# Optimization experiments

Measured on AMD Instinct MI355X. Metric: run time of the kernel, lower is better.

## Reference

```python
import jax, jax.numpy as jnp
import numpy as np

NEG = -1e30  # effective -inf in log space, fp32-safe


def _ctc_loss(logp, labels, label_lens):
    """Sum of per-sequence CTC negative log-likelihoods (blank=0).

    logp: [T, B, V] log-softmax over vocab; labels: [U, B] int (pad=1);
    label_lens: [B]. All sequences use full T frames (act_lens = T).
    """
    T, B, V = logp.shape
    U = labels.shape[0]
    S = 2 * U + 1  # blank-interleaved extended label length
    lab = labels.T  # [B, U]
    ext = jnp.zeros((B, S), dtype=jnp.int32).at[:, 1::2].set(lab.astype(jnp.int32))
    # s-2 transition allowed only for non-blank positions with ext[s] != ext[s-2]
    allow = jnp.concatenate(
        [jnp.zeros((B, 2), bool), (ext[:, 2:] != 0) & (ext[:, 2:] != ext[:, :-2])],
        axis=1,
    )  # [B, S]
    # emission log-probs gathered once: [T, B, S]
    emit = jnp.take_along_axis(logp, jnp.broadcast_to(ext[None], (T, B, S)), axis=2)
    # alpha_0: only s=0 (blank) and s=1 (first label) reachable
    alpha0 = jnp.where(jnp.arange(S)[None, :] < 2, emit[0], NEG)

    def step(alpha, emit_t):
        s1 = jnp.pad(alpha[:, :-1], ((0, 0), (1, 0)), constant_values=NEG)
        s2 = jnp.where(allow, jnp.pad(alpha[:, :-2], ((0, 0), (2, 0)), constant_values=NEG), NEG)
        alpha = jnp.logaddexp(jnp.logaddexp(alpha, s1), s2) + emit_t
        return alpha, None

    alphaT, _ = jax.lax.scan(step, alpha0, emit[1:])
    end = 2 * label_lens  # [B] index of final blank in ext
    idx = jnp.stack([end, end - 1], axis=1)  # [B, 2]
    ll = jax.nn.logsumexp(jnp.take_along_axis(alphaT, idx, axis=1), axis=1)
    return -jnp.sum(ll)  # size_average=False -> sum over batch


def setup_inputs() -> dict:
    T, B, D, NVOC, U = 800, 16, 256, 4000, 100
    V = NVOC + 1  # +1 for blank (index 0)
    key = jax.random.key(0)
    kc, kw, ky, kl = jax.random.split(key, 4)
    ctx = jax.random.normal(kc, (T, B, D), jnp.float32)
    W = jax.random.normal(kw, (D, V), jnp.float32) * 0.02
    b = jnp.zeros((V,), jnp.float32)
    lens = jax.random.randint(kl, (B,), 50, U + 1)
    raw = jax.random.randint(ky, (U, B), 2, V)  # labels in [2, n_vocab]
    y = jnp.where(jnp.arange(U)[:, None] < lens[None, :], raw, 1).astype(jnp.int32)
    return {"ctx": ctx, "y": y, "W": W, "b": b}


def reference(ctx, y, W, b):
    # hid2prob: linear projection to n_vocab+1 logits
    out = jnp.einsum('tbd,dv->tbv', ctx, W) + b  # [T, B, V]
    logps = jax.nn.log_softmax(out, axis=-1)
    label_lens = jnp.sum(y != 1, axis=0)  # pad token is 1
    loss = _ctc_loss(logps, y, label_lens)
    return loss, logps
```

## Files before the change

kernel.cpp:

```cpp
#include <hip/hip_runtime.h>
#include <hip/hip_bf16.h>
#include <stdint.h>

#define T_ 800
#define B_ 16
#define D_ 256
#define V_ 4001
#define U_ 100
#define S_ 201
#define SP 204
#define M_ (T_*B_)
#define NEGF (-1e30f)
#define L2E 1.4426950408889634f
#define LN2 0.6931471805599453f

typedef __bf16 bf16;
typedef __bf16 bf16x8 __attribute__((ext_vector_type(8)));
typedef float f32x4 __attribute__((ext_vector_type(4)));

#define A_OFF     0
#define WT_OFF    6553600
#define EMIT_OFF  8650752
#define EXT_OFF   19095552
#define AMASK_OFF 19108608
#define LENS_OFF  19121664

__global__ void prep_kernel(const int* __restrict__ y, float* __restrict__ out,
                            int* __restrict__ ext, float* __restrict__ amask,
                            int* __restrict__ lens) {
  const int tid = threadIdx.x;
  if (tid == 0) out[0] = 0.f;
  if (tid < B_) {
    int cnt = 0;
    for (int u = 0; u < U_; u++) cnt += (y[u*B_ + tid] != 1) ? 1 : 0;
    lens[tid] = cnt;
  }
  for (int idx = tid; idx < B_*SP; idx += 256) {
    int b = idx / SP, s = idx - b*SP;
    int e = 0;
    if (s < S_ && (s & 1)) e = y[((s-1) >> 1)*B_ + b];
    ext[idx] = e;
    float am = NEGF;
    if ((s & 1) && s >= 3 && s < S_) {
      int e2 = y[((s-3) >> 1)*B_ + b];
      if (e != 0 && e != e2) am = 0.f;
    }
    amask[idx] = am;
  }
}

__global__ void cast_a_kernel(const float* __restrict__ ctx, bf16* __restrict__ A) {
  int i = blockIdx.x * blockDim.x + threadIdx.x;
  float4 v = ((const float4*)ctx)[i];
  union { bf16 h[4]; uint2 u; } p;
  p.h[0] = (bf16)v.x; p.h[1] = (bf16)v.y; p.h[2] = (bf16)v.z; p.h[3] = (bf16)v.w;
  ((uint2*)A)[i] = p.u;
}

__global__ void trans_w_kernel(const float* __restrict__ W, bf16* __restrict__ Wt) {
  __shared__ float tile[32][33];
  const int c = threadIdx.x & 31, r = threadIdx.x >> 5;
  const int n0 = blockIdx.x * 32, k0 = blockIdx.y * 32;
  for (int rr = r; rr < 32; rr += 8) {
    int n = n0 + c;
    tile[rr][c] = (n < V_) ? W[(size_t)(k0+rr)*V_ + n] : 0.f;
  }
  __syncthreads();
  for (int rr = r; rr < 32; rr += 8) {
    Wt[(size_t)(n0+rr)*D_ + k0 + c] = (bf16)tile[c][rr];
  }
}

__global__ __launch_bounds__(256) void gemm_kernel(
    const bf16* __restrict__ A, const bf16* __restrict__ Wt,
    const float* __restrict__ bias, float* __restrict__ out) {
  __shared__ bf16 smA[128*72];
  __shared__ bf16 smB[128*72];
  const int tid = threadIdx.x;
  const int l = tid & 63, w = tid >> 6;
  const int wr = w >> 1, wc = w & 1;
  const int n0 = blockIdx.x * 128, m0 = blockIdx.y * 128;

  f32x4 acc[4][4];
#pragma unroll
  for (int i = 0; i < 4; i++)
#pragma unroll
    for (int j = 0; j < 4; j++) acc[i][j] = (f32x4){0.f, 0.f, 0.f, 0.f};

  for (int kt = 0; kt < 4; kt++) {
#pragma unroll
    for (int r = 0; r < 4; r++) {
      int j = (w*4 + r)*64 + l;
      int row = j >> 3, c = j & 7;
      bf16x8 va = *(const bf16x8*)(A  + (size_t)(m0+row)*D_ + kt*64 + c*8);
      bf16x8 vb = *(const bf16x8*)(Wt + (size_t)(n0+row)*D_ + kt*64 + c*8);
      *(bf16x8*)((char*)smA + row*144 + (c<<4)) = va;
      *(bf16x8*)((char*)smB + row*144 + (c<<4)) = vb;
    }
    __syncthreads();
#pragma unroll
    for (int ks = 0; ks < 2; ks++) {
      bf16x8 af[4], bfr[4];
      const int cidx = ks*4 + (l >> 4);
#pragma unroll
      for (int t = 0; t < 4; t++) {
        int arow = wr*64 + t*16 + (l & 15);
        af[t]  = *(const bf16x8*)((const char*)smA + arow*144 + (cidx<<4));
        int brow = wc*64 + t*16 + (l & 15);
        bfr[t] = *(const bf16x8*)((const char*)smB + brow*144 + (cidx<<4));
      }
#pragma unroll
      for (int i = 0; i < 4; i++)
#pragma unroll
        for (int j = 0; j < 4; j++)
          acc[i][j] = __builtin_amdgcn_mfma_f32_16x16x32_bf16(af[i], bfr[j], acc[i][j], 0, 0, 0);
    }
    __syncthreads();
  }
#pragma unroll
  for (int j = 0; j < 4; j++) {
    int gn = n0 + wc*64 + j*16 + (l & 15);
    if (gn < V_) {
      float bv = bias[gn];
#pragma unroll
      for (int i = 0; i < 4; i++) {
        int rbase = m0 + wr*64 + i*16 + ((l >> 4) << 2);
#pragma unroll
        for (int rg = 0; rg < 4; rg++) {
          out[1 + (size_t)(rbase + rg)*V_ + gn] = acc[i][j][rg] + bv;
        }
      }
    }
  }
}

__global__ __launch_bounds__(256) void softmax_gather_kernel(
    float* __restrict__ out, const int* __restrict__ ext, float* __restrict__ emit) {
  __shared__ float srow[4096];
  __shared__ float red[8];
  const int row = blockIdx.x, tid = threadIdx.x;
  float* rp = out + 1 + (size_t)row * V_;
  float v[16];
  float mx = NEGF;
#pragma unroll
  for (int j = 0; j < 16; j++) {
    int c = tid + j*256;
    v[j] = (c < V_) ? rp[c] : NEGF;
    mx = fmaxf(mx, v[j]);
  }
#pragma unroll
  for (int o = 32; o > 0; o >>= 1) mx = fmaxf(mx, __shfl_xor(mx, o));
  if ((tid & 63) == 0) red[tid >> 6] = mx;
  __syncthreads();
  mx = fmaxf(fmaxf(red[0], red[1]), fmaxf(red[2], red[3]));
  float sm = 0.f;
#pragma unroll
  for (int j = 0; j < 16; j++) sm += exp2f((v[j] - mx) * L2E);
#pragma unroll
  for (int o = 32; o > 0; o >>= 1) sm += __shfl_xor(sm, o);
  if ((tid & 63) == 0) red[4 + (tid >> 6)] = sm;
  __syncthreads();
  const float lse = mx + log2f(red[4] + red[5] + red[6] + red[7]) * LN2;
#pragma unroll
  for (int j = 0; j < 16; j++) {
    int c = tid + j*256;
    if (c < V_) {
      float lp = v[j] - lse;
      rp[c] = lp;
      srow[c] = lp;
    }
  }
  __syncthreads();
  if (tid < SP) {
    float e = NEGF;
    if (tid < S_) e = srow[ext[(row & (B_-1))*SP + tid]] * L2E;
    emit[((size_t)(row & (B_-1))*T_ + (row >> 4))*SP + tid] = e;
  }
}

__device__ __forceinline__ float dpp_shr1(float x) {
  int r = __builtin_amdgcn_update_dpp(__float_as_int(NEGF), __float_as_int(x),
                                      0x138 , 0xf, 0xf, false);
  return __int_as_float(r);
}

__device__ __forceinline__ float lae3(float a, float b, float c) {
  float m  = fmaxf(fmaxf(a, b), c);
  float md = __builtin_amdgcn_fmed3f(a, b, c);
  float mn = fminf(fminf(a, b), c);
  float s = 1.0f + __builtin_amdgcn_exp2f(md - m) + __builtin_amdgcn_exp2f(mn - m);
  return m + __builtin_amdgcn_logf(s);
}

#define CH 32

__global__ __launch_bounds__(256) void alpha_kernel(
    const float* __restrict__ emit, const float* __restrict__ amp,
    const int* __restrict__ lens, float* __restrict__ out) {
  __shared__ float ring[2][CH][256];
  __shared__ float aS[256];
  const int b = blockIdx.x;
  const int tid = threadIdx.x;
  const int wv = tid >> 6, l = tid & 63;
  const bool act = (l < 51);
  const float* ebase = emit + (size_t)b*T_*SP;
  const float4 NEG4 = make_float4(NEGF, NEGF, NEGF, NEGF);

  float a0 = NEGF, a1 = NEGF, a2 = NEGF, a3 = NEGF;
  float4 am = NEG4;

  if (wv == 0) {
    if (act) am = *(const float4*)(amp + b*SP + 4*l);
    if (l == 0) { a0 = ebase[0]; a1 = ebase[1]; }
  } else if (act) {
    for (int j = wv - 1; j < CH; j += 3) {
      float4 v = *(const float4*)(ebase + (size_t)(1 + j)*SP + 4*l);
      *(float4*)&ring[0][j][4*l] = v;
    }
  }
  __syncthreads();

  auto step = [&](const float* slot) {
    float4 cur = act ? *(const float4*)(slot + 4*l) : NEG4;
    float sh1 = dpp_shr1(a3);
    float sh2 = dpp_shr1(a2);
    float n0 = lae3(a0, sh1, sh2 + am.x) + cur.x;
    float n1 = lae3(a1, a0,  sh1 + am.y) + cur.y;
    float n2 = lae3(a2, a1,  a0  + am.z) + cur.z;
    float n3 = lae3(a3, a2,  a1  + am.w) + cur.w;
    a0 = n0; a1 = n1; a2 = n2; a3 = n3;
  };

  for (int c = 0; c < 24; c++) {
    if (wv) {
      if (act) {
        const int base_t = 1 + (c + 1)*CH;
        float* dst = &ring[(c + 1) & 1][0][0];
        for (int j = wv - 1; j < CH; j += 3) {
          int t = base_t + j;
          if (t > T_ - 1) t = T_ - 1;
          float4 v = *(const float4*)(ebase + (size_t)t*SP + 4*l);
          *(float4*)(dst + j*256 + 4*l) = v;
        }
      }
    } else {
      const float* src = &ring[c & 1][0][0];
#pragma unroll
      for (int j = 0; j < CH; j++) step(src + j*256);
    }
    __syncthreads();
  }
  if (wv == 0) {
    const float* src = &ring[0][0][0];
#pragma unroll
    for (int j = 0; j < 31; j++) step(src + j*256);
    aS[4*l+0] = a0; aS[4*l+1] = a1; aS[4*l+2] = a2; aS[4*l+3] = a3;
  }
  __syncthreads();
  if (tid == 0) {
    int e = 2 * lens[b];
    float la = aS[e], lb = aS[e-1];
    float m = fmaxf(la, lb);
    float ll2 = m + log2f(exp2f(la - m) + exp2f(lb - m));
    atomicAdd(out, -ll2 * LN2);
  }
}

extern "C" void kernel_launch(void* const* d_in, const int* in_sizes, int n_in,
                              void* d_out, int out_size, void* d_ws, size_t ws_size,
                              hipStream_t stream) {
  const float* ctx  = (const float*)d_in[0];
  const int*   y    = (const int*)  d_in[1];
  const float* W    = (const float*)d_in[2];
  const float* bias = (const float*)d_in[3];
  float* out = (float*)d_out;
  char* ws = (char*)d_ws;
  bf16*  A     = (bf16*) (ws + A_OFF);
  bf16*  Wt    = (bf16*) (ws + WT_OFF);
  float* emit  = (float*)(ws + EMIT_OFF);
  int*   ext   = (int*)  (ws + EXT_OFF);
  float* amp   = (float*)(ws + AMASK_OFF);
  int*   lens  = (int*)  (ws + LENS_OFF);

  hipLaunchKernelGGL(prep_kernel, dim3(1), dim3(256), 0, stream, y, out, ext, amp, lens);
  hipLaunchKernelGGL(cast_a_kernel, dim3(3200), dim3(256), 0, stream, ctx, A);
  hipLaunchKernelGGL(trans_w_kernel, dim3(128, 8), dim3(256), 0, stream, W, Wt);
  hipLaunchKernelGGL(gemm_kernel, dim3(32, 100), dim3(256), 0, stream, A, Wt, bias, out);
  hipLaunchKernelGGL(softmax_gather_kernel, dim3(12800), dim3(256), 0, stream, out, ext, emit);
  hipLaunchKernelGGL(alpha_kernel, dim3(16), dim3(256), 0, stream, emit, amp, lens, out);
}
```

Measured before the change: 468.2 us.

## Restructure CTC alpha kernel, swizzle GEMM blocks, use fast exp/log intrinsics

The alpha recursion now runs one wavefront per batch sequence, 8 sequences per block, and prefetches emissions straight from global memory into registers two steps ahead. This replaces the old LDS ring buffer with its producer wavefronts and block-wide barriers. Even extended positions (blanks) now use a two-term logaddexp, since the skip transition can never be allowed there. The GEMM remaps block IDs to change the order tiles are scheduled across the XCDs, and the softmax uses hardware exp2/log intrinsics. The risks are that global load latency inside the serial recursion is hidden only by the small prefetch, and that 16 sequences now occupy just 2 blocks.

Result: slower. 551.1 us (+17.7%).

```diff
diff --git a/kernel.cpp b/kernel.cpp
--- a/kernel.cpp
+++ b/kernel.cpp
@@ -79,7 +79,9 @@
   const int tid = threadIdx.x;
   const int l = tid & 63, w = tid >> 6;
   const int wr = w >> 1, wc = w & 1;
-  const int n0 = blockIdx.x * 128, m0 = blockIdx.y * 128;
+  const int orig = blockIdx.y * 32 + blockIdx.x;
+  const int virt = (orig & 7) * 400 + (orig >> 3);
+  const int n0 = (virt & 31) * 128, m0 = (virt >> 5) * 128;
 
   f32x4 acc[4][4];
 #pragma unroll
@@ -155,12 +157,12 @@
   mx = fmaxf(fmaxf(red[0], red[1]), fmaxf(red[2], red[3]));
   float sm = 0.f;
 #pragma unroll
-  for (int j = 0; j < 16; j++) sm += exp2f((v[j] - mx) * L2E);
+  for (int j = 0; j < 16; j++) sm += __builtin_amdgcn_exp2f((v[j] - mx) * L2E);
 #pragma unroll
   for (int o = 32; o > 0; o >>= 1) sm += __shfl_xor(sm, o);
   if ((tid & 63) == 0) red[4 + (tid >> 6)] = sm;
   __syncthreads();
-  const float lse = mx + log2f(red[4] + red[5] + red[6] + red[7]) * LN2;
+  const float lse = mx + __builtin_amdgcn_logf(red[4] + red[5] + red[6] + red[7]) * LN2;
 #pragma unroll
   for (int j = 0; j < 16; j++) {
     int c = tid + j*256;
@@ -192,74 +194,55 @@
   return m + __builtin_amdgcn_logf(s);
 }
 
-#define CH 32
-
-__global__ __launch_bounds__(256) void alpha_kernel(
+__device__ __forceinline__ float lae2(float a, float b) {
+  float m  = fmaxf(a, b);
+  float mn = fminf(a, b);
+  float s = 1.0f + __builtin_amdgcn_exp2f(mn - m);
+  return m + __builtin_amdgcn_logf(s);
+}
+
+__global__ __launch_bounds__(512) void alpha_kernel(
     const float* __restrict__ emit, const float* __restrict__ amp,
     const int* __restrict__ lens, float* __restrict__ out) {
-  __shared__ float ring[2][CH][256];
-  __shared__ float aS[256];
-  const int b = blockIdx.x;
-  const int tid = threadIdx.x;
-  const int wv = tid >> 6, l = tid & 63;
+  __shared__ float aS[8][256];
+  const int wv = threadIdx.x >> 6, l = threadIdx.x & 63;
+  const int b = blockIdx.x * 8 + wv;
   const bool act = (l < 51);
   const float* ebase = emit + (size_t)b*T_*SP;
   const float4 NEG4 = make_float4(NEGF, NEGF, NEGF, NEGF);
 
+  float4 am = act ? *(const float4*)(amp + b*SP + 4*l) : NEG4;
   float a0 = NEGF, a1 = NEGF, a2 = NEGF, a3 = NEGF;
-  float4 am = NEG4;
-
-  if (wv == 0) {
-    if (act) am = *(const float4*)(amp + b*SP + 4*l);
-    if (l == 0) { a0 = ebase[0]; a1 = ebase[1]; }
-  } else if (act) {
-    for (int j = wv - 1; j < CH; j += 3) {
-      float4 v = *(const float4*)(ebase + (size_t)(1 + j)*SP + 4*l);
-      *(float4*)&ring[0][j][4*l] = v;
-    }
-  }
-  __syncthreads();
-
-  auto step = [&](const float* slot) {
-    float4 cur = act ? *(const float4*)(slot + 4*l) : NEG4;
+  if (l == 0) { a0 = ebase[0]; a1 = ebase[1]; }
+
+  auto ld = [&](int t) -> float4 {
+    return *(const float4*)(ebase + (size_t)t*SP + 4*l);
+  };
+  auto step = [&](float4 cur) {
     float sh1 = dpp_shr1(a3);
-    float sh2 = dpp_shr1(a2);
-    float n0 = lae3(a0, sh1, sh2 + am.x) + cur.x;
-    float n1 = lae3(a1, a0,  sh1 + am.y) + cur.y;
-    float n2 = lae3(a2, a1,  a0  + am.z) + cur.z;
-    float n3 = lae3(a3, a2,  a1  + am.w) + cur.w;
+    float n0 = lae2(a0, sh1)              + cur.x;
+    float n1 = lae3(a1, a0, sh1 + am.y)   + cur.y;
+    float n2 = lae2(a2, a1)               + cur.z;
+    float n3 = lae3(a3, a2, a1  + am.w)   + cur.w;
     a0 = n0; a1 = n1; a2 = n2; a3 = n3;
   };
 
-  for (int c = 0; c < 24; c++) {
-    if (wv) {
-      if (act) {
-        const int base_t = 1 + (c + 1)*CH;
-        float* dst = &ring[(c + 1) & 1][0][0];
-        for (int j = wv - 1; j < CH; j += 3) {
-          int t = base_t + j;
-          if (t > T_ - 1) t = T_ - 1;
-          float4 v = *(const float4*)(ebase + (size_t)t*SP + 4*l);
-          *(float4*)(dst + j*256 + 4*l) = v;
-        }
-      }
-    } else {
-      const float* src = &ring[c & 1][0][0];
-#pragma unroll
-      for (int j = 0; j < CH; j++) step(src + j*256);
-    }
-    __syncthreads();
-  }
-  if (wv == 0) {
-    const float* src = &ring[0][0][0];
-#pragma unroll
-    for (int j = 0; j < 31; j++) step(src + j*256);
-    aS[4*l+0] = a0; aS[4*l+1] = a1; aS[4*l+2] = a2; aS[4*l+3] = a3;
-  }
-  __syncthreads();
-  if (tid == 0) {
+  float4 c0 = ld(1), c1 = ld(2);
+  for (int k = 0; k < 398; k++) {
+    float4 p0 = c0; c0 = ld(2*k + 3);
+    step(p0);
+    float4 p1 = c1; c1 = ld(2*k + 4);
+    step(p1);
+  }
+  step(c0);
+  step(c1);
+  step(ld(799));
+
+  aS[wv][4*l+0] = a0; aS[wv][4*l+1] = a1;
+  aS[wv][4*l+2] = a2; aS[wv][4*l+3] = a3;
+  if (l == 0) {
     int e = 2 * lens[b];
-    float la = aS[e], lb = aS[e-1];
+    float la = aS[wv][e], lb = aS[wv][e-1];
     float m = fmaxf(la, lb);
     float ll2 = m + log2f(exp2f(la - m) + exp2f(lb - m));
     atomicAdd(out, -ll2 * LN2);
@@ -287,5 +270,5 @@
   hipLaunchKernelGGL(trans_w_kernel, dim3(128, 8), dim3(256), 0, stream, W, Wt);
   hipLaunchKernelGGL(gemm_kernel, dim3(32, 100), dim3(256), 0, stream, A, Wt, bias, out);
   hipLaunchKernelGGL(softmax_gather_kernel, dim3(12800), dim3(256), 0, stream, out, ext, emit);
-  hipLaunchKernelGGL(alpha_kernel, dim3(16), dim3(256), 0, stream, emit, amp, lens, out);
-}
+  hipLaunchKernelGGL(alpha_kernel, dim3(2), dim3(512), 0, stream, emit, amp, lens, out);
+}
```
